# Optimization experiments

Hardware: AMD Instinct MI355X
Metric: run time of the kernel (lower is better)

The kernel has to match this reference:

```python
import jax, jax.numpy as jnp
import numpy as np
from jax import lax

START_IDX = 510
END_IDX = 511
SEQ_LEN = 32768
NUM_TAGS = 512
NEG_FILL = -10000.0


def setup_inputs() -> dict:
    key = jax.random.key(0)
    k1, k2 = jax.random.split(key)
    unary = jax.random.normal(k1, (SEQ_LEN, 1, NUM_TAGS), dtype=jnp.float32)
    trans = jax.random.normal(k2, (1, NUM_TAGS, NUM_TAGS), dtype=jnp.float32)
    lengths = jnp.full((1,), SEQ_LEN, dtype=jnp.int64)
    return {"unary": unary, "trans": trans, "lengths": lengths}


def reference(unary, trans, lengths):
    # unary: [T, 1, N] -> [T, N]; trans: [1, N, N] -> [N, N], trans[j, k] = score(k -> j)
    u = unary[:, 0, :]
    tr = trans[0]
    n_tags = tr.shape[0]

    # alphas[start_idx] = 0, else -10000
    alphas0 = jnp.where(jnp.arange(n_tags) == START_IDX,
                        jnp.float32(0.0), jnp.float32(NEG_FILL))

    def step(alphas, u_t):
        scores = alphas[None, :] + tr          # [N, N]: to-tag j, from-tag k
        best = jnp.argmax(scores, axis=1)      # backpointers [N]
        vit = jnp.max(scores, axis=1)          # [N]
        return vit + u_t, best

    alphas, backptrs = lax.scan(step, alphas0, u)   # backptrs: [T, N] int

    terminal = alphas + tr[END_IDX, :]
    best_tag = jnp.argmax(terminal)
    path_score = terminal[best_tag]

    # traceback: tag_{t-1} = backptrs[t][tag_t]
    def tb(tag, bp_t):
        return bp_t[tag], tag

    _, path = lax.scan(tb, best_tag, backptrs, reverse=True)  # [T]
    return path[:, None], path_score
```

## Files before the change

### kernel.cpp

```cpp
#include <hip/hip_runtime.h>
#include <cstdint>
#include <cstddef>

#define SEQ       32768
#define NT        512
#define START_TAG 510
#define END_TAG   511
#define NEGF      -10000.0f
#define KCH       64
#define NCH       (SEQ / KCH)

#define NBLK      16
#define TPB       1024
#define CPB       32

#define BP_BYTES  ((size_t)SEQ * NT * sizeof(unsigned short))
#define M_OFF     (BP_BYTES)
#define M_BYTES   ((size_t)NCH * NT * sizeof(unsigned short))
#define BD_OFF    (M_OFF + M_BYTES)
#define BD_BYTES  ((size_t)NCH * sizeof(int))
#define AG_OFF    ((BD_OFF + BD_BYTES + 63) & ~(size_t)63)

__global__ __launch_bounds__(NT) void init_k(unsigned long long* AgP) {
    const int t = threadIdx.x;
    const float a0 = (t == START_TAG) ? 0.0f : NEGF;
    AgP[t]      = (unsigned long long)__float_as_uint(a0);
    AgP[NT + t] = ((unsigned long long)0xFFFFFFFFu << 32)
                | (unsigned long long)__float_as_uint(NEGF);
}

__global__ __launch_bounds__(TPB) void viterbi_fwd(const float* __restrict__ u,
                                                   const float* __restrict__ trans,
                                                   unsigned short* __restrict__ bp,
                                                   unsigned long long* AgP) {
    __shared__ float4 abuf[2][NT / 4];

    const int tid  = threadIdx.x;
    const int wv   = tid >> 6;
    const int lane = tid & 63;
    const int gp   = lane >> 5;
    const int m    = lane & 31;
    const int b    = (int)blockIdx.x;
    const int jb   = b * CPB + wv * 2;
    const int j    = jb + gp;
    const int i0   = 16 * m;

    const float4 t0 = *(const float4*)&trans[(size_t)j * NT + i0];
    const float4 t1 = *(const float4*)&trans[(size_t)j * NT + i0 + 4];
    const float4 t2 = *(const float4*)&trans[(size_t)j * NT + i0 + 8];
    const float4 t3 = *(const float4*)&trans[(size_t)j * NT + i0 + 12];

    float uval = 0.0f;
    if (m == 0) uval = u[j];

    for (int t = 0; t < SEQ; ++t) {
        const int par = t & 1;

        float unext = 0.0f;
        const int tn = (t + 1 < SEQ) ? (t + 1) : t;
        if (m == 0) unext = u[(size_t)tn * NT + j];

        if (wv == 0) {
            const unsigned long long* sb = AgP + (size_t)par * NT + lane;
            unsigned long long va[8];
            const unsigned expt = (unsigned)t;
            for (;;) {
                bool ok = true;
                #pragma unroll
                for (int r = 0; r < 8; ++r) {
                    va[r] = __hip_atomic_load(&sb[r * 64], __ATOMIC_RELAXED,
                                              __HIP_MEMORY_SCOPE_AGENT);
                    ok &= ((unsigned)(va[r] >> 32) == expt);
                }
                if (ok) break;
            }
            float* awf = (float*)&abuf[par][0];
            #pragma unroll
            for (int r = 0; r < 8; ++r) {
                const int i    = r * 64 + lane;
                const int phys = i ^ (((i >> 5) & 7) << 2);
                awf[phys] = __uint_as_float((unsigned)va[r]);
            }
        }
        __syncthreads();

        float v0, v1, v2, v3; int x0, x1, x2, x3; float s;
        {   const int ib = i0;      const int pb = ib ^ (((ib >> 5) & 7) << 2);
            const float4 a = abuf[par][pb >> 2];
            v0 = a.x + t0.x; x0 = ib;
            s = a.y + t0.y; if (s > v0) { v0 = s; x0 = ib + 1; }
            s = a.z + t0.z; if (s > v0) { v0 = s; x0 = ib + 2; }
            s = a.w + t0.w; if (s > v0) { v0 = s; x0 = ib + 3; } }
        {   const int ib = i0 + 4;  const int pb = ib ^ (((ib >> 5) & 7) << 2);
            const float4 a = abuf[par][pb >> 2];
            v1 = a.x + t1.x; x1 = ib;
            s = a.y + t1.y; if (s > v1) { v1 = s; x1 = ib + 1; }
            s = a.z + t1.z; if (s > v1) { v1 = s; x1 = ib + 2; }
            s = a.w + t1.w; if (s > v1) { v1 = s; x1 = ib + 3; } }
        {   const int ib = i0 + 8;  const int pb = ib ^ (((ib >> 5) & 7) << 2);
            const float4 a = abuf[par][pb >> 2];
            v2 = a.x + t2.x; x2 = ib;
            s = a.y + t2.y; if (s > v2) { v2 = s; x2 = ib + 1; }
            s = a.z + t2.z; if (s > v2) { v2 = s; x2 = ib + 2; }
            s = a.w + t2.w; if (s > v2) { v2 = s; x2 = ib + 3; } }
        {   const int ib = i0 + 12; const int pb = ib ^ (((ib >> 5) & 7) << 2);
            const float4 a = abuf[par][pb >> 2];
            v3 = a.x + t3.x; x3 = ib;
            s = a.y + t3.y; if (s > v3) { v3 = s; x3 = ib + 1; }
            s = a.z + t3.z; if (s > v3) { v3 = s; x3 = ib + 2; }
            s = a.w + t3.w; if (s > v3) { v3 = s; x3 = ib + 3; } }
        if (v1 > v0) { v0 = v1; x0 = x1; }
        if (v3 > v2) { v2 = v3; x2 = x3; }
        if (v2 > v0) { v0 = v2; x0 = x2; }
        float bv = v0; int bi = x0;

        #pragma unroll
        for (int h = 1; h <= 16; h <<= 1) {
            const float ov = __shfl_xor(bv, h);
            const int   oi = __shfl_xor(bi, h);
            if (ov > bv || (ov == bv && oi < bi)) { bv = ov; bi = oi; }
        }

        if (m == 0) {
            const float na = bv + uval;
            const unsigned long long pk =
                ((unsigned long long)(unsigned)(t + 1) << 32)
                | (unsigned long long)__float_as_uint(na);
            __hip_atomic_store(&AgP[(size_t)((t + 1) & 1) * NT + j], pk,
                               __ATOMIC_RELAXED, __HIP_MEMORY_SCOPE_AGENT);
        }

        const int oi1 = __shfl(bi, 32);
        if (lane == 0) {
            *(unsigned*)&bp[(size_t)t * NT + jb] =
                (unsigned)(bi & 0xFFFF) | ((unsigned)oi1 << 16);
        }
        uval = unext;
    }
}

__global__ __launch_bounds__(NT) void mbuild_k(const unsigned short* __restrict__ bp,
                                               unsigned short* __restrict__ M) {
    __shared__ unsigned short R[2][NT];
    const int c = (int)blockIdx.x, j = threadIdx.x;
    const size_t base = (size_t)c * KCH * NT;
    R[0][j] = bp[base + j];
    int cb = 0;
    for (int t = 1; t < KCH; ++t) {
        const unsigned short r = bp[base + (size_t)t * NT + j];
        __syncthreads();
        R[cb ^ 1][j] = R[cb][r];
        cb ^= 1;
    }
    __syncthreads();
    M[(size_t)c * NT + j] = R[cb][j];
}

__global__ __launch_bounds__(NT) void chase_k(const unsigned long long* __restrict__ AgP,
                                              const float* __restrict__ tr,
                                              const unsigned short* __restrict__ M,
                                              int* __restrict__ boundary,
                                              float* __restrict__ out) {
    __shared__ float sv[NT];
    __shared__ int   si[NT];
    const int j = threadIdx.x;
    sv[j] = __uint_as_float((unsigned)AgP[j]) + tr[(size_t)END_TAG * NT + j];
    si[j] = j;
    __syncthreads();
    for (int off = NT / 2; off > 0; off >>= 1) {
        if (j < off) {
            const float a = sv[j], b = sv[j + off];
            if (b > a || (b == a && si[j + off] < si[j])) { sv[j] = b; si[j] = si[j + off]; }
        }
        __syncthreads();
    }
    if (j == 0) {
        out[SEQ] = sv[0];
        int tag = si[0];
        boundary[NCH - 1] = tag;
        for (int c = NCH - 1; c >= 1; --c) {
            tag = (int)M[(size_t)c * NT + tag];
            boundary[c - 1] = tag;
        }
    }
}

__global__ __launch_bounds__(64) void traceback_k(const unsigned short* __restrict__ bp,
                                                  const int* __restrict__ boundary,
                                                  float* __restrict__ out) {
    if (threadIdx.x != 0) return;
    const int c    = (int)blockIdx.x;
    int       tag  = boundary[c];
    const int tend = (c + 1) * KCH - 1;
    out[tend] = (float)tag;
    for (int t = tend - 1; t >= c * KCH; --t) {
        tag = (int)bp[(size_t)(t + 1) * NT + tag];
        out[t] = (float)tag;
    }
}

extern "C" void kernel_launch(void* const* d_in, const int* in_sizes, int n_in,
                              void* d_out, int out_size, void* d_ws, size_t ws_size,
                              hipStream_t stream) {
    const float* unary = (const float*)d_in[0];
    const float* trans = (const float*)d_in[1];
    float* out = (float*)d_out;
    char*  ws  = (char*)d_ws;

    unsigned short*     bp       = (unsigned short*)ws;
    unsigned short*     M        = (unsigned short*)(ws + M_OFF);
    int*                boundary = (int*)(ws + BD_OFF);
    unsigned long long* AgP      = (unsigned long long*)(ws + AG_OFF);
    (void)in_sizes; (void)n_in; (void)out_size; (void)ws_size;

    init_k<<<1, NT, 0, stream>>>(AgP);
    viterbi_fwd<<<NBLK, TPB, 0, stream>>>(unary, trans, bp, AgP);
    mbuild_k<<<NCH, NT, 0, stream>>>(bp, M);
    chase_k<<<1, NT, 0, stream>>>(AgP, trans, M, boundary, out);
    traceback_k<<<NCH, 64, 0, stream>>>(bp, boundary, out);
}
```

Measured before the change: 69.36 ms.

## Pin forward Viterbi blocks to a single XCC and poll with sc0 loads

Launches 512 small blocks. Each block reads its XCC id through s_getreg and registers in a global rendezvous, and only the first 64 blocks on the most populated XCC do the work. The intent is to keep all inter-block step synchronization traffic inside one XCC's L2 rather than crossing dies. The spin-wait uses inline-asm sc0 loads that may hit the local cache, with a full agent-scope atomic load every 32nd iteration. Risks: the global rendezvous deadlocks if not all 512 blocks are co-resident, and stale sc0 reads could slow the polling, although correctness is kept by the periodic atomic loads.

Result: slower. 273.6 ms (+294.4%).

```diff
diff --git a/kernel.cpp b/kernel.cpp
--- a/kernel.cpp
+++ b/kernel.cpp
@@ -10,9 +10,12 @@
 #define KCH       64
 #define NCH       (SEQ / KCH)
 
-#define NBLK      16
-#define TPB       1024
-#define CPB       32
+#define NBLK      512
+#define TPB       256
+#define PFIX      64
+#define CPB       8
+
+#define XCC_GETREG_IMM 63508
 
 #define BP_BYTES  ((size_t)SEQ * NT * sizeof(unsigned short))
 #define M_OFF     (BP_BYTES)
@@ -20,28 +23,53 @@
 #define BD_OFF    (M_OFF + M_BYTES)
 #define BD_BYTES  ((size_t)NCH * sizeof(int))
 #define AG_OFF    ((BD_OFF + BD_BYTES + 63) & ~(size_t)63)
-
-__global__ __launch_bounds__(NT) void init_k(unsigned long long* AgP) {
+#define AG_BYTES  ((size_t)2 * NT * sizeof(unsigned long long))
+#define RS_OFF    (AG_OFF + AG_BYTES)
+
+__global__ __launch_bounds__(NT) void init_k(unsigned long long* AgP, int* ros) {
     const int t = threadIdx.x;
     const float a0 = (t == START_TAG) ? 0.0f : NEGF;
     AgP[t]      = (unsigned long long)__float_as_uint(a0);
     AgP[NT + t] = ((unsigned long long)0xFFFFFFFFu << 32)
                 | (unsigned long long)__float_as_uint(NEGF);
+    if (t < 9) ros[t] = 0;
 }
 
 __global__ __launch_bounds__(TPB) void viterbi_fwd(const float* __restrict__ u,
                                                    const float* __restrict__ trans,
                                                    unsigned short* __restrict__ bp,
-                                                   unsigned long long* AgP) {
+                                                   unsigned long long* AgP,
+                                                   int* ros) {
     __shared__ float4 abuf[2][NT / 4];
+    __shared__ int sh_rank;
+
+    if (threadIdx.x == 0) {
+        const unsigned xcc = __builtin_amdgcn_s_getreg(XCC_GETREG_IMM) & 7u;
+        const int rank = __hip_atomic_fetch_add(&ros[xcc], 1, __ATOMIC_RELAXED,
+                                                __HIP_MEMORY_SCOPE_AGENT);
+        __hip_atomic_fetch_add(&ros[8], 1, __ATOMIC_RELEASE,
+                               __HIP_MEMORY_SCOPE_AGENT);
+        while (__hip_atomic_load(&ros[8], __ATOMIC_ACQUIRE,
+                                 __HIP_MEMORY_SCOPE_AGENT) < NBLK) {}
+        int best = 0, bc = 0;
+        #pragma unroll
+        for (int x = 0; x < 8; ++x) {
+            const int c = __hip_atomic_load(&ros[x], __ATOMIC_RELAXED,
+                                            __HIP_MEMORY_SCOPE_AGENT);
+            if (c > bc) { bc = c; best = x; }
+        }
+        sh_rank = ((int)xcc == best && rank < PFIX) ? rank : -1;
+    }
+    __syncthreads();
+    const int rank = sh_rank;
+    if (rank < 0) return;
 
     const int tid  = threadIdx.x;
     const int wv   = tid >> 6;
     const int lane = tid & 63;
     const int gp   = lane >> 5;
     const int m    = lane & 31;
-    const int b    = (int)blockIdx.x;
-    const int jb   = b * CPB + wv * 2;
+    const int jb   = rank * CPB + wv * 2;
     const int j    = jb + gp;
     const int i0   = 16 * m;
 
@@ -62,25 +90,54 @@
 
         if (wv == 0) {
             const unsigned long long* sb = AgP + (size_t)par * NT + lane;
-            unsigned long long va[8];
+            unsigned long long v0, v1, v2, v3, v4, v5, v6, v7;
             const unsigned expt = (unsigned)t;
-            for (;;) {
-                bool ok = true;
-                #pragma unroll
-                for (int r = 0; r < 8; ++r) {
-                    va[r] = __hip_atomic_load(&sb[r * 64], __ATOMIC_RELAXED,
-                                              __HIP_MEMORY_SCOPE_AGENT);
-                    ok &= ((unsigned)(va[r] >> 32) == expt);
+            int it = 0;
+            bool ok;
+            do {
+                if ((it++ & 31) != 31) {
+                    asm volatile(
+                        "global_load_dwordx2 %0, %8, off sc0\n\t"
+                        "global_load_dwordx2 %1, %8, off offset:512 sc0\n\t"
+                        "global_load_dwordx2 %2, %8, off offset:1024 sc0\n\t"
+                        "global_load_dwordx2 %3, %8, off offset:1536 sc0\n\t"
+                        "global_load_dwordx2 %4, %8, off offset:2048 sc0\n\t"
+                        "global_load_dwordx2 %5, %8, off offset:2560 sc0\n\t"
+                        "global_load_dwordx2 %6, %8, off offset:3072 sc0\n\t"
+                        "global_load_dwordx2 %7, %8, off offset:3584 sc0\n\t"
+                        "s_waitcnt vmcnt(0)"
+                        : "=&v"(v0), "=&v"(v1), "=&v"(v2), "=&v"(v3),
+                          "=&v"(v4), "=&v"(v5), "=&v"(v6), "=&v"(v7)
+                        : "v"(sb) : "memory");
+                } else {
+                    v0 = __hip_atomic_load(&sb[0],   __ATOMIC_RELAXED, __HIP_MEMORY_SCOPE_AGENT);
+                    v1 = __hip_atomic_load(&sb[64],  __ATOMIC_RELAXED, __HIP_MEMORY_SCOPE_AGENT);
+                    v2 = __hip_atomic_load(&sb[128], __ATOMIC_RELAXED, __HIP_MEMORY_SCOPE_AGENT);
+                    v3 = __hip_atomic_load(&sb[192], __ATOMIC_RELAXED, __HIP_MEMORY_SCOPE_AGENT);
+                    v4 = __hip_atomic_load(&sb[256], __ATOMIC_RELAXED, __HIP_MEMORY_SCOPE_AGENT);
+                    v5 = __hip_atomic_load(&sb[320], __ATOMIC_RELAXED, __HIP_MEMORY_SCOPE_AGENT);
+                    v6 = __hip_atomic_load(&sb[384], __ATOMIC_RELAXED, __HIP_MEMORY_SCOPE_AGENT);
+                    v7 = __hip_atomic_load(&sb[448], __ATOMIC_RELAXED, __HIP_MEMORY_SCOPE_AGENT);
                 }
-                if (ok) break;
-            }
+                ok = ((unsigned)(v0 >> 32) == expt)
+                   & ((unsigned)(v1 >> 32) == expt)
+                   & ((unsigned)(v2 >> 32) == expt)
+                   & ((unsigned)(v3 >> 32) == expt)
+                   & ((unsigned)(v4 >> 32) == expt)
+                   & ((unsigned)(v5 >> 32) == expt)
+                   & ((unsigned)(v6 >> 32) == expt)
+                   & ((unsigned)(v7 >> 32) == expt);
+            } while (!ok);
+
             float* awf = (float*)&abuf[par][0];
-            #pragma unroll
-            for (int r = 0; r < 8; ++r) {
-                const int i    = r * 64 + lane;
-                const int phys = i ^ (((i >> 5) & 7) << 2);
-                awf[phys] = __uint_as_float((unsigned)va[r]);
-            }
+            { const int i_ = lane;       awf[i_ ^ (((i_ >> 5) & 7) << 2)] = __uint_as_float((unsigned)v0); }
+            { const int i_ = 64 + lane;  awf[i_ ^ (((i_ >> 5) & 7) << 2)] = __uint_as_float((unsigned)v1); }
+            { const int i_ = 128 + lane; awf[i_ ^ (((i_ >> 5) & 7) << 2)] = __uint_as_float((unsigned)v2); }
+            { const int i_ = 192 + lane; awf[i_ ^ (((i_ >> 5) & 7) << 2)] = __uint_as_float((unsigned)v3); }
+            { const int i_ = 256 + lane; awf[i_ ^ (((i_ >> 5) & 7) << 2)] = __uint_as_float((unsigned)v4); }
+            { const int i_ = 320 + lane; awf[i_ ^ (((i_ >> 5) & 7) << 2)] = __uint_as_float((unsigned)v5); }
+            { const int i_ = 384 + lane; awf[i_ ^ (((i_ >> 5) & 7) << 2)] = __uint_as_float((unsigned)v6); }
+            { const int i_ = 448 + lane; awf[i_ ^ (((i_ >> 5) & 7) << 2)] = __uint_as_float((unsigned)v7); }
         }
         __syncthreads();
 
@@ -211,10 +268,11 @@
     unsigned short*     M        = (unsigned short*)(ws + M_OFF);
     int*                boundary = (int*)(ws + BD_OFF);
     unsigned long long* AgP      = (unsigned long long*)(ws + AG_OFF);
+    int*                ros      = (int*)(ws + RS_OFF);
     (void)in_sizes; (void)n_in; (void)out_size; (void)ws_size;
 
-    init_k<<<1, NT, 0, stream>>>(AgP);
-    viterbi_fwd<<<NBLK, TPB, 0, stream>>>(unary, trans, bp, AgP);
+    init_k<<<1, NT, 0, stream>>>(AgP, ros);
+    viterbi_fwd<<<NBLK, TPB, 0, stream>>>(unary, trans, bp, AgP, ros);
     mbuild_k<<<NCH, NT, 0, stream>>>(bp, M);
     chase_k<<<1, NT, 0, stream>>>(AgP, trans, M, boundary, out);
     traceback_k<<<NCH, 64, 0, stream>>>(bp, boundary, out);
```

## Spread Viterbi forward over more small blocks and double-buffer flag polling

Applied to the files above, without the earlier changes.

Moves the persistent forward kernel from 16 blocks of 1024 threads to 64 blocks of 256 threads, so each block handles 8 target tags. The spin-wait on the per-step alpha flags now keeps two batches of atomic loads in flight, so one round of polling is outstanding while the previous round is checked. The aim is to cut the per-step cross-block synchronisation latency and the intra-block barrier cost. In exchange, 64 blocks now poll the shared alpha array every step, which adds memory traffic, and the pipelined polling issues extra loads.

Measured after the change: 75.45 ms. 1.09x slower.

```diff
diff --git a/kernel.cpp b/kernel.cpp
--- a/kernel.cpp
+++ b/kernel.cpp
@@ -10,9 +10,9 @@
 #define KCH       64
 #define NCH       (SEQ / KCH)
 
-#define NBLK      16
-#define TPB       1024
-#define CPB       32
+#define NBLK      64
+#define TPB       256
+#define CPB       8
 
 #define BP_BYTES  ((size_t)SEQ * NT * sizeof(unsigned short))
 #define M_OFF     (BP_BYTES)
@@ -62,18 +62,46 @@
 
         if (wv == 0) {
             const unsigned long long* sb = AgP + (size_t)par * NT + lane;
-            unsigned long long va[8];
+            unsigned long long A[8], B[8], va[8];
             const unsigned expt = (unsigned)t;
+
+            #pragma unroll
+            for (int r = 0; r < 8; ++r)
+                A[r] = __hip_atomic_load(&sb[r * 64], __ATOMIC_RELAXED,
+                                         __HIP_MEMORY_SCOPE_AGENT);
             for (;;) {
-                bool ok = true;
                 #pragma unroll
-                for (int r = 0; r < 8; ++r) {
-                    va[r] = __hip_atomic_load(&sb[r * 64], __ATOMIC_RELAXED,
-                                              __HIP_MEMORY_SCOPE_AGENT);
-                    ok &= ((unsigned)(va[r] >> 32) == expt);
+                for (int r = 0; r < 8; ++r)
+                    B[r] = __hip_atomic_load(&sb[r * 64], __ATOMIC_RELAXED,
+                                             __HIP_MEMORY_SCOPE_AGENT);
+                {
+                    bool ok = true;
+                    #pragma unroll
+                    for (int r = 0; r < 8; ++r)
+                        ok &= ((unsigned)(A[r] >> 32) == expt);
+                    if (ok) {
+                        #pragma unroll
+                        for (int r = 0; r < 8; ++r) va[r] = A[r];
+                        break;
+                    }
                 }
-                if (ok) break;
+                #pragma unroll
+                for (int r = 0; r < 8; ++r)
+                    A[r] = __hip_atomic_load(&sb[r * 64], __ATOMIC_RELAXED,
+                                             __HIP_MEMORY_SCOPE_AGENT);
+                {
+                    bool ok = true;
+                    #pragma unroll
+                    for (int r = 0; r < 8; ++r)
+                        ok &= ((unsigned)(B[r] >> 32) == expt);
+                    if (ok) {
+                        #pragma unroll
+                        for (int r = 0; r < 8; ++r) va[r] = B[r];
+                        break;
+                    }
+                }
             }
+
             float* awf = (float*)&abuf[par][0];
             #pragma unroll
             for (int r = 0; r < 8; ++r) {
```
